# Performance work log

Measured on AMD Instinct MI355X. Metric: run time of the kernel, lower is better.

The kernel has to match this reference:

```python
import jax, jax.numpy as jnp
import numpy as np

WIN = (8, 8)          # window height/width -> seq_len n = 64
GAMMA = 16            # channel groups (s)
BLOCKS = 1024         # num_blocks == number of windows w
GATE_DIM = 256        # dim // chunks
EPS = 1e-5


def _rel_indices(win):
    # Quadratic relative-position features [n, n, 3] = (dx, dy, dx^2+dy^2)
    w, h = win
    ind = np.arange(h)[None, :] - np.arange(w)[:, None]            # (w, h)
    indx = np.tile(ind, (h, w))                                    # (n, n)
    indy = np.repeat(np.repeat(ind, h, axis=0), w, axis=1).T       # (n, n)
    indd = indx ** 2 + indy ** 2
    return jnp.asarray(np.stack([indx, indy, indd], axis=-1), dtype=jnp.float32)


def setup_inputs() -> dict:
    key = jax.random.key(0)
    k0, k1, k2 = jax.random.split(key, 3)
    b = 4
    n = WIN[0] * WIN[1]
    return {
        "x": jax.random.normal(k0, (b, BLOCKS, n, 2 * GATE_DIM), dtype=jnp.float32),
        "norm_weight": jnp.ones((GATE_DIM,), jnp.float32),
        "norm_bias": jnp.zeros((GATE_DIM,), jnp.float32),
        "attention_centers": 0.01 * jax.random.normal(k1, (BLOCKS * GAMMA, 2), jnp.float32),
        "attention_spreads": 1.0 + 0.01 * jax.random.normal(k2, (BLOCKS * GAMMA,), jnp.float32),
        "token_proj_n_bias": jnp.zeros((BLOCKS, n, 1), jnp.float32),
    }


def reference(x, norm_weight, norm_bias, attention_centers, attention_spreads, token_proj_n_bias):
    b, w, n, d = x.shape
    # chunk into gate halves: u mixed spatially, v is the gate
    u, v = jnp.split(x, 2, axis=-1)                                # [b,w,n,gd] each
    # LayerNorm over channel dim (biased variance, as torch)
    mean = u.mean(-1, keepdims=True)
    var = u.var(-1, keepdims=True)
    u = (u - mean) * jax.lax.rsqrt(var + EPS) * norm_weight + norm_bias
    # quadratic positional weights (QuaMap.forward_qua_pos)
    mu1, mu2 = attention_centers[:, 0], attention_centers[:, 1]
    a = attention_spreads ** 2
    pos_proj = jnp.stack([a * mu1, a * mu2, -0.5 * jnp.ones_like(mu1)], axis=-1)  # [g*w, 3]
    rel = _rel_indices(WIN)                                        # [n,n,3]
    pos_score = jnp.einsum('mnd,bd->bmn', rel, pos_proj)           # [g*w, n, n]
    win_weight = jax.nn.softmax(pos_score, axis=-1)
    # rearrange '(s b) m n -> b m n s' with s=gamma
    win_weight = win_weight.reshape(GAMMA, w, n, n).transpose(1, 2, 3, 0)  # [w,m,n,s]
    # rearrange 'b w n (v s) -> b w n v s'
    vdim = u.shape[-1] // GAMMA
    uu = u.reshape(b, w, n, vdim, GAMMA)
    # windowed spatial mixing + per-window bias
    mixed = jnp.einsum('wmns,bwnvs->bwmvs', win_weight, uu)
    mixed = mixed + token_proj_n_bias[None, :, :, None, :]          # [1,w,n,1,1]
    u = mixed.reshape(b, w, n, vdim * GAMMA)
    return u * v
```

## Files before the change

### kernel.cpp

```cpp
#include <hip/hip_runtime.h>
#include <cstdint>

#if __has_builtin(__builtin_amdgcn_exp2f)
#define EXP2F(x) __builtin_amdgcn_exp2f(x)
#else
#define EXP2F(x) exp2f(x)
#endif

typedef _Float16 half8 __attribute__((ext_vector_type(8)));
typedef _Float16 half4 __attribute__((ext_vector_type(4)));
typedef float    f32x4 __attribute__((ext_vector_type(4)));


__global__ __launch_bounds__(512, 4) void sgating_kernel(
    const float* __restrict__ x,
    const float* __restrict__ norm_w,
    const float* __restrict__ norm_b,
    const float* __restrict__ centers,
    const float* __restrict__ spreads,
    const float* __restrict__ tbias,
    float* __restrict__ out)
{
    __shared__ __align__(16) float smem[12288];
    _Float16* Us = (_Float16*)smem;
    float*    Qm = smem + 8192;

    const int t     = threadIdx.x;
    const int wv    = t >> 6;
    const int lane  = t & 63;
    const int bw    = blockIdx.x;
    const int w_idx = bw & 1023;
    const size_t xbase = (size_t)bw * (64 * 512);
    const size_t obase = (size_t)bw * (64 * 256);

    half4 vreg[8];

    {
        const float4 w4 = *(const float4*)(norm_w + lane * 4);
        const float4 b4 = *(const float4*)(norm_b + lane * 4);
        half8 uar[4];
#pragma unroll
        for (int r = 0; r < 8; ++r) {
            const int n = r * 8 + wv;
            const float* rowp = x + xbase + (size_t)n * 512 + lane * 4;
            const float4 u  = *(const float4*)(rowp);
            const float4 vv = *(const float4*)(rowp + 256);
            vreg[r][0] = (_Float16)vv.x; vreg[r][1] = (_Float16)vv.y;
            vreg[r][2] = (_Float16)vv.z; vreg[r][3] = (_Float16)vv.w;
            float s  = u.x + u.y + u.z + u.w;
            float sq = u.x*u.x + u.y*u.y + u.z*u.z + u.w*u.w;
#pragma unroll
            for (int off = 1; off < 64; off <<= 1) {
                s  += __shfl_xor(s, off);
                sq += __shfl_xor(sq, off);
            }
            const float mean = s * (1.0f/256.0f);
            const float var  = sq * (1.0f/256.0f) - mean*mean;
            const float rstd = rsqrtf(var + 1e-5f);
            uar[0][r] = (_Float16)((u.x - mean)*rstd*w4.x + b4.x);
            uar[1][r] = (_Float16)((u.y - mean)*rstd*w4.y + b4.y);
            uar[2][r] = (_Float16)((u.z - mean)*rstd*w4.z + b4.z);
            uar[3][r] = (_Float16)((u.w - mean)*rstd*w4.w + b4.w);
        }
#pragma unroll
        for (int j = 0; j < 4; ++j) {
            const int d  = lane * 4 + j;
            const int s  = d & 15;
            const int vd = d >> 4;
            const int qb = wv ^ (vd & 7);
            *(half8*)(Us + (s << 10) + (vd << 6) + (qb << 3)) = uar[j];
        }
    }
    __syncthreads();

    const int m16 = lane & 15;
    const int g   = lane >> 4;
    const float LOG2E = 1.4426950408889634f;
    const float C2    = 0.72134752044448f;
    const float mx  = (float)(m16 & 7);
    const float myb = (float)(m16 >> 3);
    const int sA = wv, sB = wv + 8;

    float bias4[4];
#pragma unroll
    for (int nt = 0; nt < 4; ++nt)
        bias4[nt] = tbias[w_idx * 64 + nt * 16 + m16];

    float    exfA[2], exfB[2];
    _Float16 exhA[2], exhB[2];
    half8 EYA_[2], EYB_[2];
    {
        const int hbA = (sA << 10) | w_idx;
        const int hbB = (sB << 10) | w_idx;
        float aq = spreads[hbA]; aq *= aq;
        const float axlA = aq * centers[2*hbA]     * LOG2E;
        const float aylA = aq * centers[2*hbA + 1] * LOG2E;
        aq = spreads[hbB]; aq *= aq;
        const float axlB = aq * centers[2*hbB]     * LOG2E;
        const float aylB = aq * centers[2*hbB + 1] * LOG2E;
#pragma unroll
        for (int kt = 0; kt < 2; ++kt) {
            const float dx = (float)(g + 4*kt) - mx;
            const float eA = EXP2F(dx * fmaf(-C2, dx, axlA));
            const float eB = EXP2F(dx * fmaf(-C2, dx, axlB));
            exfA[kt] = eA; exhA[kt] = (_Float16)eA;
            exfB[kt] = eB; exhB[kt] = (_Float16)eB;
        }
#pragma unroll
        for (int i = 0; i < 16; ++i) {
            const float dy = (float)(i - 7) + myb;
            const _Float16 eA = (i < 14) ? (_Float16)EXP2F(dy * fmaf(-C2, dy, aylA)) : (_Float16)0.f;
            const _Float16 eB = (i < 14) ? (_Float16)EXP2F(dy * fmaf(-C2, dy, aylB)) : (_Float16)0.f;
            if (i < 8) { EYA_[0][i] = eA; EYB_[0][i] = eB; }
            else       { EYA_[1][i-8] = eA; EYB_[1][i-8] = eB; }
        }
    }

#define EYAT(I) ((I) < 8 ? EYA_[0][(I)] : EYA_[1][(I)-8])
#define EYBT(I) ((I) < 8 ? EYB_[0][(I)] : EYB_[1][(I)-8])

#define CQ(NT, vOutA, vOutB) do {                                              \
    f32x4 aA = (f32x4){0.f,0.f,0.f,0.f};                                       \
    f32x4 aB = (f32x4){0.f,0.f,0.f,0.f};                                       \
    half8 eyA8, eyB8;                                                          \
    float syA = 0.f, syB = 0.f;                                                \
    _Pragma("unroll") for (int j = 0; j < 8; ++j) {                            \
        const _Float16 ea = EYAT(2*(NT)+7-j);                                  \
        const _Float16 eb = EYBT(2*(NT)+7-j);                                  \
        eyA8[j] = ea; eyB8[j] = eb;                                            \
        syA += (float)ea; syB += (float)eb;                                    \
    }                                                                          \
    _Pragma("unroll") for (int kt = 0; kt < 2; ++kt) {                         \
        const int qb = (g + 4*kt) ^ (m16 & 7);                                 \
        const half8 uA = *(const half8*)(Us + (sA<<10) + (m16<<6) + (qb<<3));  \
        const half8 uB = *(const half8*)(Us + (sB<<10) + (m16<<6) + (qb<<3));  \
        half8 wA, wB;                                                          \
        _Pragma("unroll") for (int j = 0; j < 8; ++j) {                        \
            wA[j] = eyA8[j] * exhA[kt];                                        \
            wB[j] = eyB8[j] * exhB[kt];                                        \
        }                                                                      \
        aA = __builtin_amdgcn_mfma_f32_16x16x32_f16(uA, wA, aA, 0, 0, 0);      \
        aB = __builtin_amdgcn_mfma_f32_16x16x32_f16(uB, wB, aB, 0, 0, 0);      \
    }                                                                          \
    float rA = (exfA[0] + exfA[1]) * syA;                                      \
    rA += __shfl_xor(rA, 16); rA += __shfl_xor(rA, 32);                        \
    float rB = (exfB[0] + exfB[1]) * syB;                                      \
    rB += __shfl_xor(rB, 16); rB += __shfl_xor(rB, 32);                        \
    const float iA = 1.0f / rA;                                                \
    const float iB = 1.0f / rB;                                                \
    const float bm = bias4[(NT)];                                              \
    _Pragma("unroll") for (int j = 0; j < 4; ++j) {                            \
        vOutA[j] = aA[j]*iA + bm;                                              \
        vOutB[j] = aB[j]*iB + bm;                                              \
    }                                                                          \
} while (0)

#define WRITEQ(vA_, vB_) do {                                                  \
    const int swz = (m16 & 7) << 2;                                            \
    *(f32x4*)(Qm + (m16<<8) + ((sA*16 + g*4) ^ swz)) = vA_;                    \
    *(f32x4*)(Qm + (m16<<8) + ((sB*16 + g*4) ^ swz)) = vB_;                    \
} while (0)

#define EPIK(NT, K) do {                                                       \
    const int mr  = wv + 8*(K);                                                \
    const int m   = (NT)*16 + mr;                                              \
    const int c4  = lane * 4;                                                  \
    const int vd  = c4 >> 4;                                                   \
    const int s0  = c4 & 15;                                                   \
    const int sw2 = (m & 7) << 2;                                              \
    f32x4 mxv;                                                                 \
    mxv[0] = Qm[(mr<<8) + ((((s0+0)<<4)+vd) ^ sw2)];                           \
    mxv[1] = Qm[(mr<<8) + ((((s0+1)<<4)+vd) ^ sw2)];                           \
    mxv[2] = Qm[(mr<<8) + ((((s0+2)<<4)+vd) ^ sw2)];                           \
    mxv[3] = Qm[(mr<<8) + ((((s0+3)<<4)+vd) ^ sw2)];                           \
    const half4 vh = vreg[2*(NT)+(K)];                                         \
    f32x4 o;                                                                   \
    o[0] = mxv[0] * (float)vh[0]; o[1] = mxv[1] * (float)vh[1];                \
    o[2] = mxv[2] * (float)vh[2]; o[3] = mxv[3] * (float)vh[3];                \
    __builtin_nontemporal_store(o, (f32x4*)(out + obase + m*256 + c4));        \
} while (0)

    f32x4 cA, cB, nA2, nB2;
    CQ(0, cA, cB);

    WRITEQ(cA, cB);
    __syncthreads();
    CQ(1, nA2, nB2);
    EPIK(0, 0); EPIK(0, 1);
    __syncthreads();
    cA = nA2; cB = nB2;

    WRITEQ(cA, cB);
    __syncthreads();
    CQ(2, nA2, nB2);
    EPIK(1, 0); EPIK(1, 1);
    __syncthreads();
    cA = nA2; cB = nB2;

    WRITEQ(cA, cB);
    __syncthreads();
    CQ(3, nA2, nB2);
    EPIK(2, 0); EPIK(2, 1);
    __syncthreads();
    cA = nA2; cB = nB2;

    WRITEQ(cA, cB);
    __syncthreads();
    EPIK(3, 0); EPIK(3, 1);
}

extern "C" void kernel_launch(void* const* d_in, const int* in_sizes, int n_in,
                              void* d_out, int out_size, void* d_ws, size_t ws_size,
                              hipStream_t stream) {
    const float* x       = (const float*)d_in[0];
    const float* norm_w  = (const float*)d_in[1];
    const float* norm_b  = (const float*)d_in[2];
    const float* centers = (const float*)d_in[3];
    const float* spreads = (const float*)d_in[4];
    const float* tbias   = (const float*)d_in[5];
    float* out = (float*)d_out;

    const int nbw = in_sizes[0] / (64 * 512);
    hipLaunchKernelGGL(sgating_kernel, dim3(nbw), dim3(512), 0, stream,
                       x, norm_w, norm_b, centers, spreads, tbias, out);
}
```

Before: 156.3 us.

## Make kernel persistent over batch with prefetch of next window's u rows

The grid shrinks to 1024 workgroups, each looping over the batch dimension for its window, so the per-window softmax weights and bias are computed once and reused. The u half of the next iteration is prefetched into registers while the current one is processed, and the v gate is loaded just in time in fp32 rather than converted to fp16 up front. Barriers become raw s_barrier calls with only an LDS wait. In exchange there are fewer workgroups and therefore less parallelism, and register pressure rises from the prefetch buffers.

```diff
diff --git a/kernel.cpp b/kernel.cpp
--- a/kernel.cpp
+++ b/kernel.cpp
@@ -8,9 +8,13 @@
 #endif
 
 typedef _Float16 half8 __attribute__((ext_vector_type(8)));
-typedef _Float16 half4 __attribute__((ext_vector_type(4)));
 typedef float    f32x4 __attribute__((ext_vector_type(4)));
 
+
+#define BARRIER() do {                                        \
+    asm volatile("s_waitcnt lgkmcnt(0)" ::: "memory");        \
+    __builtin_amdgcn_s_barrier();                             \
+} while (0)
 
 __global__ __launch_bounds__(512, 4) void sgating_kernel(
     const float* __restrict__ x,
@@ -19,7 +23,8 @@
     const float* __restrict__ centers,
     const float* __restrict__ spreads,
     const float* __restrict__ tbias,
-    float* __restrict__ out)
+    float* __restrict__ out,
+    int nit)
 {
     __shared__ __align__(16) float smem[12288];
     _Float16* Us = (_Float16*)smem;
@@ -28,50 +33,8 @@
     const int t     = threadIdx.x;
     const int wv    = t >> 6;
     const int lane  = t & 63;
-    const int bw    = blockIdx.x;
-    const int w_idx = bw & 1023;
-    const size_t xbase = (size_t)bw * (64 * 512);
-    const size_t obase = (size_t)bw * (64 * 256);
-
-    half4 vreg[8];
-
-    {
-        const float4 w4 = *(const float4*)(norm_w + lane * 4);
-        const float4 b4 = *(const float4*)(norm_b + lane * 4);
-        half8 uar[4];
-#pragma unroll
-        for (int r = 0; r < 8; ++r) {
-            const int n = r * 8 + wv;
-            const float* rowp = x + xbase + (size_t)n * 512 + lane * 4;
-            const float4 u  = *(const float4*)(rowp);
-            const float4 vv = *(const float4*)(rowp + 256);
-            vreg[r][0] = (_Float16)vv.x; vreg[r][1] = (_Float16)vv.y;
-            vreg[r][2] = (_Float16)vv.z; vreg[r][3] = (_Float16)vv.w;
-            float s  = u.x + u.y + u.z + u.w;
-            float sq = u.x*u.x + u.y*u.y + u.z*u.z + u.w*u.w;
-#pragma unroll
-            for (int off = 1; off < 64; off <<= 1) {
-                s  += __shfl_xor(s, off);
-                sq += __shfl_xor(sq, off);
-            }
-            const float mean = s * (1.0f/256.0f);
-            const float var  = sq * (1.0f/256.0f) - mean*mean;
-            const float rstd = rsqrtf(var + 1e-5f);
-            uar[0][r] = (_Float16)((u.x - mean)*rstd*w4.x + b4.x);
-            uar[1][r] = (_Float16)((u.y - mean)*rstd*w4.y + b4.y);
-            uar[2][r] = (_Float16)((u.z - mean)*rstd*w4.z + b4.z);
-            uar[3][r] = (_Float16)((u.w - mean)*rstd*w4.w + b4.w);
-        }
-#pragma unroll
-        for (int j = 0; j < 4; ++j) {
-            const int d  = lane * 4 + j;
-            const int s  = d & 15;
-            const int vd = d >> 4;
-            const int qb = wv ^ (vd & 7);
-            *(half8*)(Us + (s << 10) + (vd << 6) + (qb << 3)) = uar[j];
-        }
-    }
-    __syncthreads();
+    const int wg    = blockIdx.x;
+    const int w_idx = wg & 1023;
 
     const int m16 = lane & 15;
     const int g   = lane >> 4;
@@ -80,6 +43,9 @@
     const float mx  = (float)(m16 & 7);
     const float myb = (float)(m16 >> 3);
     const int sA = wv, sB = wv + 8;
+
+    const float4 w4 = *(const float4*)(norm_w + lane * 4);
+    const float4 b4 = *(const float4*)(norm_b + lane * 4);
 
     float bias4[4];
 #pragma unroll
@@ -161,7 +127,12 @@
     *(f32x4*)(Qm + (m16<<8) + ((sB*16 + g*4) ^ swz)) = vB_;                    \
 } while (0)
 
-#define EPIK(NT, K) do {                                                       \
+#define VLOAD(NT, V0, V1) do {                                                 \
+    V0 = *(const f32x4*)(x + xbase + (size_t)(16*(NT)+wv)*512 + 256 + lane*4); \
+    V1 = *(const f32x4*)(x + xbase + (size_t)(16*(NT)+8+wv)*512 + 256 + lane*4);\
+} while (0)
+
+#define EPIK(NT, K, VH) do {                                                   \
     const int mr  = wv + 8*(K);                                                \
     const int m   = (NT)*16 + mr;                                              \
     const int c4  = lane * 4;                                                  \
@@ -173,40 +144,94 @@
     mxv[1] = Qm[(mr<<8) + ((((s0+1)<<4)+vd) ^ sw2)];                           \
     mxv[2] = Qm[(mr<<8) + ((((s0+2)<<4)+vd) ^ sw2)];                           \
     mxv[3] = Qm[(mr<<8) + ((((s0+3)<<4)+vd) ^ sw2)];                           \
-    const half4 vh = vreg[2*(NT)+(K)];                                         \
     f32x4 o;                                                                   \
-    o[0] = mxv[0] * (float)vh[0]; o[1] = mxv[1] * (float)vh[1];                \
-    o[2] = mxv[2] * (float)vh[2]; o[3] = mxv[3] * (float)vh[3];                \
+    o[0] = mxv[0] * (VH)[0]; o[1] = mxv[1] * (VH)[1];                          \
+    o[2] = mxv[2] * (VH)[2]; o[3] = mxv[3] * (VH)[3];                          \
     __builtin_nontemporal_store(o, (f32x4*)(out + obase + m*256 + c4));        \
 } while (0)
 
-    f32x4 cA, cB, nA2, nB2;
-    CQ(0, cA, cB);
-
-    WRITEQ(cA, cB);
-    __syncthreads();
-    CQ(1, nA2, nB2);
-    EPIK(0, 0); EPIK(0, 1);
-    __syncthreads();
-    cA = nA2; cB = nB2;
-
-    WRITEQ(cA, cB);
-    __syncthreads();
-    CQ(2, nA2, nB2);
-    EPIK(1, 0); EPIK(1, 1);
-    __syncthreads();
-    cA = nA2; cB = nB2;
-
-    WRITEQ(cA, cB);
-    __syncthreads();
-    CQ(3, nA2, nB2);
-    EPIK(2, 0); EPIK(2, 1);
-    __syncthreads();
-    cA = nA2; cB = nB2;
-
-    WRITEQ(cA, cB);
-    __syncthreads();
-    EPIK(3, 0); EPIK(3, 1);
+    f32x4 un[8];
+    {
+        const size_t xb0 = (size_t)wg * (64 * 512);
+#pragma unroll
+        for (int r = 0; r < 8; ++r)
+            un[r] = *(const f32x4*)(x + xb0 + (size_t)(r*8 + wv)*512 + lane*4);
+    }
+
+    for (int it = 0; it < nit; ++it) {
+        const int bw = wg + (it << 10);
+        const size_t xbase = (size_t)bw * (64 * 512);
+        const size_t obase = (size_t)bw * (64 * 256);
+
+        {
+            half8 uar[4];
+#pragma unroll
+            for (int r = 0; r < 8; ++r) {
+                const f32x4 u = un[r];
+                float s  = u[0] + u[1] + u[2] + u[3];
+                float sq = u[0]*u[0] + u[1]*u[1] + u[2]*u[2] + u[3]*u[3];
+#pragma unroll
+                for (int off = 1; off < 64; off <<= 1) {
+                    s  += __shfl_xor(s, off);
+                    sq += __shfl_xor(sq, off);
+                }
+                const float mean = s * (1.0f/256.0f);
+                const float var  = sq * (1.0f/256.0f) - mean*mean;
+                const float rstd = rsqrtf(var + 1e-5f);
+                uar[0][r] = (_Float16)((u[0] - mean)*rstd*w4.x + b4.x);
+                uar[1][r] = (_Float16)((u[1] - mean)*rstd*w4.y + b4.y);
+                uar[2][r] = (_Float16)((u[2] - mean)*rstd*w4.z + b4.z);
+                uar[3][r] = (_Float16)((u[3] - mean)*rstd*w4.w + b4.w);
+            }
+#pragma unroll
+            for (int j = 0; j < 4; ++j) {
+                const int d  = lane * 4 + j;
+                const int s  = d & 15;
+                const int vd = d >> 4;
+                const int qb = wv ^ (vd & 7);
+                *(half8*)(Us + (s << 10) + (vd << 6) + (qb << 3)) = uar[j];
+            }
+        }
+
+        f32x4 v0, v1, v2, v3, v4, v5, v6, v7;
+        VLOAD(0, v0, v1);
+        BARRIER();
+
+        if (it + 1 < nit) {
+            const size_t xbn = (size_t)(bw + 1024) * (64 * 512);
+#pragma unroll
+            for (int r = 0; r < 8; ++r)
+                un[r] = *(const f32x4*)(x + xbn + (size_t)(r*8 + wv)*512 + lane*4);
+        }
+
+        f32x4 cA, cB, nA2, nB2;
+        CQ(0, cA, cB);
+        WRITEQ(cA, cB);
+        BARRIER();
+
+        VLOAD(1, v2, v3);
+        CQ(1, nA2, nB2);
+        EPIK(0, 0, v0); EPIK(0, 1, v1);
+        BARRIER();
+        WRITEQ(nA2, nB2);
+        BARRIER();
+
+        VLOAD(2, v4, v5);
+        CQ(2, cA, cB);
+        EPIK(1, 0, v2); EPIK(1, 1, v3);
+        BARRIER();
+        WRITEQ(cA, cB);
+        BARRIER();
+
+        VLOAD(3, v6, v7);
+        CQ(3, nA2, nB2);
+        EPIK(2, 0, v4); EPIK(2, 1, v5);
+        BARRIER();
+        WRITEQ(nA2, nB2);
+        BARRIER();
+
+        EPIK(3, 0, v6); EPIK(3, 1, v7);
+    }
 }
 
 extern "C" void kernel_launch(void* const* d_in, const int* in_sizes, int n_in,
@@ -221,6 +246,9 @@
     float* out = (float*)d_out;
 
     const int nbw = in_sizes[0] / (64 * 512);
-    hipLaunchKernelGGL(sgating_kernel, dim3(nbw), dim3(512), 0, stream,
-                       x, norm_w, norm_b, centers, spreads, tbias, out);
+    int grid, nit;
+    if (nbw % 1024 == 0) { grid = 1024; nit = nbw / 1024; }
+    else                 { grid = nbw;  nit = 1; }
+    hipLaunchKernelGGL(sgating_kernel, dim3(grid), dim3(512), 0, stream,
+                       x, norm_w, norm_b, centers, spreads, tbias, out, nit);
 }
```

New measurement: 299.5 us. 91.7% more time.
